# Optimization experiments

Hardware: AMD Instinct MI355X
Metric: run time of the kernel (lower is better)

Reference implementation:

```python
import jax, jax.numpy as jnp
from jax import lax
import numpy as np

DN = ('NHWC', 'HWIO', 'NHWC')


def setup_inputs() -> dict:
    key = jax.random.key(0)
    ks = jax.random.split(key, 4)
    B, T, H, W, Cin, Cout, K = 4, 16, 64, 64, 32, 64, 3
    x = jax.random.normal(ks[0], (B, T, H, W, Cin), dtype=jnp.float32)
    kernel = jax.random.normal(ks[1], (K, K, Cin, 4 * Cout), dtype=jnp.float32) * 0.05
    rec_kernel = jax.random.normal(ks[2], (K, K, Cout, 4 * Cout), dtype=jnp.float32) * 0.05
    bias = jnp.zeros((4 * Cout,), dtype=jnp.float32)
    gamma = jnp.ones((Cout,), dtype=jnp.float32)
    beta = jnp.zeros((Cout,), dtype=jnp.float32)
    moving_mean = jnp.zeros((Cout,), dtype=jnp.float32)
    moving_var = jnp.ones((Cout,), dtype=jnp.float32)
    return dict(x=x, kernel=kernel, rec_kernel=rec_kernel, bias=bias,
                gamma=gamma, beta=beta, moving_mean=moving_mean, moving_var=moving_var)


def _hard_sigmoid(z):
    # Keras hard_sigmoid: clip(0.2*x + 0.5, 0, 1)
    return jnp.clip(0.2 * z + 0.5, 0.0, 1.0)


def _conv(x, w):
    return lax.conv_general_dilated(x, w, (1, 1), 'SAME', dimension_numbers=DN)


def reference(x, kernel, rec_kernel, bias, gamma, beta, moving_mean, moving_var):
    B, T, H, W, Cin = x.shape
    Cout = rec_kernel.shape[2]
    # Precompute input-to-gate convs for all timesteps at once: (B*T,H,W,4C)
    gx = _conv(x.reshape(B * T, H, W, Cin), kernel) + bias
    gx = gx.reshape(B, T, H, W, 4 * Cout).transpose(1, 0, 2, 3, 4)  # (T,B,H,W,4C)

    def step(carry, gxt):
        h, c = carry
        g = gxt + _conv(h, rec_kernel)  # (B,H,W,4C)
        i, f, cc, o = jnp.split(g, 4, axis=-1)  # Keras gate order i,f,c,o
        i = _hard_sigmoid(i)
        f = _hard_sigmoid(f)
        c = f * c + i * jnp.tanh(cc)
        h = _hard_sigmoid(o) * jnp.tanh(c)
        return (h, c), h

    h0 = jnp.zeros((B, H, W, Cout), dtype=x.dtype)
    c0 = jnp.zeros((B, H, W, Cout), dtype=x.dtype)
    _, hs = lax.scan(step, (h0, c0), gx)  # (T,B,H,W,C)
    y = hs.transpose(1, 0, 2, 3, 4)  # (B,T,H,W,C)
    # BatchNorm, inference mode (training=False), eps=1e-3
    inv = gamma * lax.rsqrt(moving_var + 1e-3)
    return y * inv + (beta - moving_mean * inv)
```

## Files before the change

### kernel.cpp

```cpp
#include <hip/hip_runtime.h>
#include <math.h>

#define B_ 4
#define T_ 16
#define H_ 64
#define W_ 64
#define CIN 32
#define CO 64
#define NG 256
#define PXS 40

typedef __attribute__((ext_vector_type(8))) short bf16x8;
typedef __attribute__((ext_vector_type(4))) float f32x4;

__device__ __forceinline__ float hsig(float z) {
    return fminf(1.f, fmaxf(0.f, 0.2f * z + 0.5f));
}

__device__ __forceinline__ float ftanh(float x) {
    float e = __builtin_amdgcn_exp2f(x * 2.8853900817779268f);
    return 1.f - 2.f * __builtin_amdgcn_rcpf(e + 1.f);
}

__device__ __forceinline__ unsigned short f2bf(float f) {
    union { float f; unsigned u; } v; v.f = f;
    unsigned r = v.u + 0x7FFFu + ((v.u >> 16) & 1u);
    return (unsigned short)(r >> 16);
}

__global__ void transform_weights(const float* __restrict__ wk,
                                  const float* __restrict__ wr,
                                  unsigned short* __restrict__ wkT,
                                  unsigned short* __restrict__ wrT)
{
    int i = blockIdx.x * 256 + threadIdx.x;
    if (i < 9 * 256 * 32) {
        int k = i & 31, n = (i >> 5) & 255, kpos = i >> 13;
        wkT[i] = f2bf(wk[(kpos * 32 + k) * 256 + n]);
    }
    if (i < 9 * 2 * 256 * 32) {
        int k = i & 31, n = (i >> 5) & 255, q = (i >> 13) & 1, kpos = i >> 14;
        wrT[i] = f2bf(wr[(kpos * 64 + q * 32 + k) * 256 + n]);
    }
}

template<bool FIRST>
__global__ __launch_bounds__(512, 2)
void convlstm_step(const float* __restrict__ x,
                   const unsigned short* __restrict__ wkT,
                   const unsigned short* __restrict__ wrT,
                   const float* __restrict__ bias,
                   const float* __restrict__ gamma,
                   const float* __restrict__ beta,
                   const float* __restrict__ mean,
                   const float* __restrict__ var,
                   const unsigned short* __restrict__ hin,
                   unsigned short* __restrict__ hout,
                   float* __restrict__ cbuf,
                   float* __restrict__ out,
                   int t)
{
    __shared__ __align__(16) unsigned short sx[6 * 18 * PXS];
    __shared__ __align__(16) unsigned short shm[2][6 * 18 * PXS];
    __shared__ __align__(16) float axx[4 * 4 * 4 * 16 * 20];

    const int tid = threadIdx.x;
    const int wv = tid >> 6, lane = tid & 63;
    const int ln = lane & 15, kg = lane >> 4;
    const bool hwave = (wv < 4);
    const int sl = wv & 3;

    const int bi = blockIdx.x;
    const int b = bi >> 6, tile = bi & 63;
    const int oy = (tile >> 2) * 4;
    const int ox = (tile & 3) * 16;

    unsigned short* sh0 = shm[0];
    unsigned short* sh1 = shm[1];

    if (!hwave) {
#pragma unroll
        for (int i = 0; i < 2; ++i) {
            int e = (tid - 256) + i * 256;
            if (e < 432) {
                int c8 = e & 3, p = e >> 2;
                int row = p / 18, col = p - row * 18;
                int gy = oy - 1 + row, gx = ox - 1 + col;
                float4 v0 = make_float4(0.f, 0.f, 0.f, 0.f), v1 = v0;
                if ((unsigned)gy < (unsigned)H_ && (unsigned)gx < (unsigned)W_) {
                    const float* p32 = &x[((((size_t)b * T_ + t) * H_ + gy) * W_ + gx) * CIN + c8 * 8];
                    v0 = *(const float4*)p32; v1 = *(const float4*)(p32 + 4);
                }
                unsigned short* d = &sx[(row * 18 + col) * PXS + c8 * 8];
                d[0] = f2bf(v0.x); d[1] = f2bf(v0.y); d[2] = f2bf(v0.z); d[3] = f2bf(v0.w);
                d[4] = f2bf(v1.x); d[5] = f2bf(v1.y); d[6] = f2bf(v1.z); d[7] = f2bf(v1.w);
            }
        }
    } else if (!FIRST) {
#pragma unroll
        for (int i = 0; i < 4; ++i) {
            int e = tid + i * 256;
            if (e < 864) {
                int o = e & 7, p = e >> 3;
                int row = p / 18, col = p - row * 18;
                int gy = oy - 1 + row, gx = ox - 1 + col;
                uint4 v = make_uint4(0u, 0u, 0u, 0u);
                if ((unsigned)gy < (unsigned)H_ && (unsigned)gx < (unsigned)W_)
                    v = *(const uint4*)&hin[(((size_t)b * H_ + gy) * W_ + gx) * CO + o * 8];
                int q = o >> 2, s4 = o & 3;
                *(uint4*)&shm[q][(row * 18 + col) * PXS + s4 * 8] = v;
            }
        }
    }

    const int nbase = sl * 16 + ln;
    const int ch = nbase;
    const unsigned short* wkp = wkT + (size_t)nbase * 32 + kg * 8;
    const unsigned short* wrp = wrT + (size_t)nbase * 32 + kg * 8;

    const int rbase = hwave ? 0 : 2;
    const float bi0 = bias[ch], bi1 = bias[64 + ch], bi2 = bias[128 + ch], bi3 = bias[192 + ch];
    const float inv = gamma[ch] * rsqrtf(var[ch] + 1e-3f);
    const float shift = beta[ch] - mean[ch] * inv;
    float cprev[2][4];
    if (!FIRST) {
#pragma unroll
        for (int rr = 0; rr < 2; ++rr)
#pragma unroll
            for (int reg = 0; reg < 4; ++reg) {
                size_t pix = ((size_t)b * H_ + oy + rbase + rr) * W_ + (ox + kg * 4 + reg);
                cprev[rr][reg] = cbuf[pix * CO + ch];
            }
    } else {
#pragma unroll
        for (int rr = 0; rr < 2; ++rr)
#pragma unroll
            for (int reg = 0; reg < 4; ++reg) cprev[rr][reg] = 0.f;
    }

    __syncthreads();

    f32x4 acc[4][4];
#pragma unroll
    for (int g = 0; g < 4; ++g)
#pragma unroll
        for (int r = 0; r < 4; ++r) acc[g][r] = (f32x4){0.f, 0.f, 0.f, 0.f};

#define XW_WP(i)  ((i) < 9 ? (wkp + (size_t)(i) * 8192) : (wrp + (size_t)(((i) - 9) * 2 + 1) * 8192))
#define XW_SB(i)  ((i) < 9 ? sx : sh1)
#define XW_KQ(i)  ((i) < 9 ? (i) : (i) - 9)
#define HW_WP(i)  ((i) < 9 ? (wrp + (size_t)((i) * 2) * 8192) : (wrp + (size_t)(((i) - 4) * 2 + 1) * 8192))
#define HW_SB(i)  ((i) < 9 ? sh0 : sh1)
#define HW_KQ(i)  ((i) < 9 ? (i) : (i) - 4)

#define LOADW(dst, wp) { const unsigned short* wp_ = (wp);        \
    dst[0] = *(const bf16x8*)(wp_);                               \
    dst[1] = *(const bf16x8*)(wp_ + 2048);                        \
    dst[2] = *(const bf16x8*)(wp_ + 4096);                        \
    dst[3] = *(const bf16x8*)(wp_ + 6144); }

#define COMPUTE(i, SBM, KQM, BUF) {                               \
    const int kq_ = KQM(i);                                       \
    const int ky_ = kq_ / 3, kx_ = kq_ - ky_ * 3;                 \
    const unsigned short* sb_ = SBM(i);                           \
    bf16x8 a[4];                                                  \
    _Pragma("unroll")                                             \
    for (int r = 0; r < 4; ++r)                                   \
        a[r] = *(const bf16x8*)&sb_[((r + ky_) * 18 + ln + kx_) * PXS + kg * 8]; \
    __builtin_amdgcn_s_setprio(1);                                \
    _Pragma("unroll")                                             \
    for (int g = 0; g < 4; ++g)                                   \
        _Pragma("unroll")                                         \
        for (int r = 0; r < 4; ++r)                               \
            acc[g][r] = __builtin_amdgcn_mfma_f32_16x16x32_bf16(a[r], BUF[g], acc[g][r], 0, 0, 0); \
    __builtin_amdgcn_s_setprio(0); }

    if (!hwave) {
        constexpr int NCX = FIRST ? 9 : 14;
        bf16x8 P0[4], P1[4], P2[4], P3[4];
        LOADW(P0, XW_WP(0)); LOADW(P1, XW_WP(1)); LOADW(P2, XW_WP(2));
#define XSTEP(i, CUR, NXT)                                        \
        if ((i) < NCX) {                                          \
            if ((i) + 3 < NCX) LOADW(NXT, XW_WP((i) + 3));        \
            COMPUTE(i, XW_SB, XW_KQ, CUR);                        \
        }
        XSTEP(0,  P0, P3)  XSTEP(1,  P1, P0)  XSTEP(2,  P2, P1)  XSTEP(3,  P3, P2)
        XSTEP(4,  P0, P3)  XSTEP(5,  P1, P0)  XSTEP(6,  P2, P1)  XSTEP(7,  P3, P2)
        XSTEP(8,  P0, P3)  XSTEP(9,  P1, P0)  XSTEP(10, P2, P1)  XSTEP(11, P3, P2)
        XSTEP(12, P0, P3)  XSTEP(13, P1, P0)
#undef XSTEP
    } else if (!FIRST) {
        constexpr int NCH = 13;
        bf16x8 P0[4], P1[4], P2[4], P3[4];
        LOADW(P0, HW_WP(0)); LOADW(P1, HW_WP(1)); LOADW(P2, HW_WP(2));
#define HSTEP(i, CUR, NXT)                                        \
        if ((i) < NCH) {                                          \
            if ((i) + 3 < NCH) LOADW(NXT, HW_WP((i) + 3));        \
            COMPUTE(i, HW_SB, HW_KQ, CUR);                        \
        }
        HSTEP(0,  P0, P3)  HSTEP(1,  P1, P0)  HSTEP(2,  P2, P1)  HSTEP(3,  P3, P2)
        HSTEP(4,  P0, P3)  HSTEP(5,  P1, P0)  HSTEP(6,  P2, P1)  HSTEP(7,  P3, P2)
        HSTEP(8,  P0, P3)  HSTEP(9,  P1, P0)  HSTEP(10, P2, P1)  HSTEP(11, P3, P2)
        HSTEP(12, P0, P3)
#undef HSTEP
    }

    if (!hwave) {
#pragma unroll
        for (int g = 0; g < 4; ++g) {
            *(f32x4*)&axx[((((sl * 4 + g) * 4 + 0) * 16) + ln) * 20 + kg * 4] = acc[g][0];
            *(f32x4*)&axx[((((sl * 4 + g) * 4 + 1) * 16) + ln) * 20 + kg * 4] = acc[g][1];
        }
    } else {
#pragma unroll
        for (int g = 0; g < 4; ++g) {
            *(f32x4*)&axx[((((sl * 4 + g) * 4 + 2) * 16) + ln) * 20 + kg * 4] = acc[g][2];
            *(f32x4*)&axx[((((sl * 4 + g) * 4 + 3) * 16) + ln) * 20 + kg * 4] = acc[g][3];
        }
    }
    __syncthreads();

#define EPILOG(R, RR) {                                                          \
        const int gy = oy + (R);                                                 \
        f32x4 av[4];                                                             \
        _Pragma("unroll")                                                        \
        for (int g = 0; g < 4; ++g) {                                            \
            f32x4 v = *(const f32x4*)&axx[((((sl * 4 + g) * 4 + (R)) * 16) + ln) * 20 + kg * 4]; \
            av[g] = acc[g][R] + v;                                               \
        }                                                                        \
        _Pragma("unroll")                                                        \
        for (int reg = 0; reg < 4; ++reg) {                                      \
            const int gx = ox + kg * 4 + reg;                                    \
            size_t pix = ((size_t)b * H_ + gy) * W_ + gx;                        \
            float ig = hsig(av[0][reg] + bi0);                                   \
            float fg = hsig(av[1][reg] + bi1);                                   \
            float cg = ftanh(av[2][reg] + bi2);                                  \
            float og = hsig(av[3][reg] + bi3);                                   \
            float cv = fg * cprev[RR][reg] + ig * cg;                            \
            float hv = og * ftanh(cv);                                           \
            cbuf[pix * CO + ch] = cv;                                            \
            hout[pix * CO + ch] = f2bf(hv);                                      \
            __builtin_nontemporal_store(hv * inv + shift,                        \
                &out[((((size_t)b * T_ + t) * H_ + gy) * W_ + gx) * CO + ch]);   \
        }                                                                        \
    }

    if (hwave) { EPILOG(0, 0) EPILOG(1, 1) }
    else       { EPILOG(2, 0) EPILOG(3, 1) }
#undef EPILOG
}

extern "C" void kernel_launch(void* const* d_in, const int* in_sizes, int n_in,
                              void* d_out, int out_size, void* d_ws, size_t ws_size,
                              hipStream_t stream)
{
    (void)in_sizes; (void)n_in; (void)out_size; (void)ws_size;
    const float* x     = (const float*)d_in[0];
    const float* wk    = (const float*)d_in[1];
    const float* wr    = (const float*)d_in[2];
    const float* bias  = (const float*)d_in[3];
    const float* gamma = (const float*)d_in[4];
    const float* beta  = (const float*)d_in[5];
    const float* mean  = (const float*)d_in[6];
    const float* var   = (const float*)d_in[7];
    float* out = (float*)d_out;

    const size_t plane = (size_t)B_ * H_ * W_ * CO;
    unsigned short* h0 = (unsigned short*)d_ws;
    unsigned short* h1 = h0 + plane;
    float* cb = (float*)(h1 + plane);
    unsigned short* wkT = (unsigned short*)(cb + plane);
    unsigned short* wrT = wkT + 9 * 256 * 32;

    transform_weights<<<576, 256, 0, stream>>>(wk, wr, wkT, wrT);

    for (int t = 0; t < T_; ++t) {
        const unsigned short* hin = (t & 1) ? h0 : h1;
        unsigned short* houtp     = (t & 1) ? h1 : h0;
        if (t == 0)
            convlstm_step<true><<<256, 512, 0, stream>>>(x, wkT, wrT, bias, gamma, beta, mean, var,
                                                         hin, houtp, cb, out, t);
        else
            convlstm_step<false><<<256, 512, 0, stream>>>(x, wkT, wrT, bias, gamma, beta, mean, var,
                                                          hin, houtp, cb, out, t);
    }
}
```

Measured before the change: 277.8 us.

## Split K-reduction across three wave groups with LDS partial-sum exchange

Changes the block from 8 to 12 waves so the 27 K-chunks (9 input-conv, 18 recurrent-conv) split evenly into three groups of 9. Partial accumulators are exchanged through a larger LDS buffer and the epilogue rows are redistributed across the groups. The explicit 3-deep software prefetch of weights is dropped in favour of straight-line chunk loads. The aim is to balance MFMA work across waves and raise wave-level parallelism per block. In exchange it uses more LDS, tighter register limits from the new launch bounds, and an uneven epilogue, since group 0 handles two rows while the others handle one.

```diff
diff --git a/kernel.cpp b/kernel.cpp
--- a/kernel.cpp
+++ b/kernel.cpp
@@ -45,7 +45,7 @@
 }
 
 template<bool FIRST>
-__global__ __launch_bounds__(512, 2)
+__global__ __launch_bounds__(768, 3)
 void convlstm_step(const float* __restrict__ x,
                    const unsigned short* __restrict__ wkT,
                    const unsigned short* __restrict__ wrT,
@@ -62,12 +62,12 @@
 {
     __shared__ __align__(16) unsigned short sx[6 * 18 * PXS];
     __shared__ __align__(16) unsigned short shm[2][6 * 18 * PXS];
-    __shared__ __align__(16) float axx[4 * 4 * 4 * 16 * 20];
+    __shared__ __align__(16) float axx[4 * 4 * 8 * 256];
 
     const int tid = threadIdx.x;
     const int wv = tid >> 6, lane = tid & 63;
     const int ln = lane & 15, kg = lane >> 4;
-    const bool hwave = (wv < 4);
+    const int wg = wv >> 2;
     const int sl = wv & 3;
 
     const int bi = blockIdx.x;
@@ -78,10 +78,10 @@
     unsigned short* sh0 = shm[0];
     unsigned short* sh1 = shm[1];
 
-    if (!hwave) {
+    if (wg == 2) {
 #pragma unroll
         for (int i = 0; i < 2; ++i) {
-            int e = (tid - 256) + i * 256;
+            int e = (tid - 512) + i * 256;
             if (e < 432) {
                 int c8 = e & 3, p = e >> 2;
                 int row = p / 18, col = p - row * 18;
@@ -98,8 +98,8 @@
         }
     } else if (!FIRST) {
 #pragma unroll
-        for (int i = 0; i < 4; ++i) {
-            int e = tid + i * 256;
+        for (int i = 0; i < 2; ++i) {
+            int e = tid + i * 512;
             if (e < 864) {
                 int o = e & 7, p = e >> 3;
                 int row = p / 18, col = p - row * 18;
@@ -113,121 +113,114 @@
         }
     }
 
-    const int nbase = sl * 16 + ln;
-    const int ch = nbase;
-    const unsigned short* wkp = wkT + (size_t)nbase * 32 + kg * 8;
-    const unsigned short* wrp = wrT + (size_t)nbase * 32 + kg * 8;
-
-    const int rbase = hwave ? 0 : 2;
+    const int ch = sl * 16 + ln;
+    const unsigned short* wkp = wkT + (size_t)ch * 32 + kg * 8;
+    const unsigned short* wrp = wrT + (size_t)ch * 32 + kg * 8;
+
     const float bi0 = bias[ch], bi1 = bias[64 + ch], bi2 = bias[128 + ch], bi3 = bias[192 + ch];
     const float inv = gamma[ch] * rsqrtf(var[ch] + 1e-3f);
     const float shift = beta[ch] - mean[ch] * inv;
-    float cprev[2][4];
+    float cpv[2][4];
+#pragma unroll
+    for (int rr = 0; rr < 2; ++rr)
+#pragma unroll
+        for (int reg = 0; reg < 4; ++reg) cpv[rr][reg] = 0.f;
     if (!FIRST) {
-#pragma unroll
-        for (int rr = 0; rr < 2; ++rr)
+        if (wg == 0) {
 #pragma unroll
             for (int reg = 0; reg < 4; ++reg) {
-                size_t pix = ((size_t)b * H_ + oy + rbase + rr) * W_ + (ox + kg * 4 + reg);
-                cprev[rr][reg] = cbuf[pix * CO + ch];
-            }
+                size_t pix0 = ((size_t)b * H_ + oy + 0) * W_ + (ox + kg * 4 + reg);
+                size_t pix1 = ((size_t)b * H_ + oy + 1) * W_ + (ox + kg * 4 + reg);
+                cpv[0][reg] = cbuf[pix0 * CO + ch];
+                cpv[1][reg] = cbuf[pix1 * CO + ch];
+            }
+        } else {
+            const int r = (wg == 1) ? 2 : 3;
+#pragma unroll
+            for (int reg = 0; reg < 4; ++reg) {
+                size_t pix = ((size_t)b * H_ + oy + r) * W_ + (ox + kg * 4 + reg);
+                cpv[0][reg] = cbuf[pix * CO + ch];
+            }
+        }
+    }
+
+    __syncthreads();
+
+    f32x4 acc[4][4];
+#pragma unroll
+    for (int g = 0; g < 4; ++g)
+#pragma unroll
+        for (int r = 0; r < 4; ++r) acc[g][r] = (f32x4){0.f, 0.f, 0.f, 0.f};
+
+#define WPTR(c) ((c) < 9 ? (wkp + (size_t)(c) * 8192) : (wrp + (size_t)((c) - 9) * 8192))
+#define SRCB(c) ((c) < 9 ? sx : ((((c) - 9) & 1) ? sh1 : sh0))
+#define KP(c)   ((c) < 9 ? (c) : (((c) - 9) >> 1))
+
+#define CHUNK(c) {                                                               \
+    const unsigned short* wp_ = WPTR(c);                                         \
+    bf16x8 w0 = *(const bf16x8*)(wp_);                                           \
+    bf16x8 w1 = *(const bf16x8*)(wp_ + 2048);                                    \
+    bf16x8 w2 = *(const bf16x8*)(wp_ + 4096);                                    \
+    bf16x8 w3 = *(const bf16x8*)(wp_ + 6144);                                    \
+    const int ky_ = KP(c) / 3, kx_ = KP(c) - (KP(c) / 3) * 3;                    \
+    const unsigned short* sb_ = SRCB(c);                                         \
+    bf16x8 a0 = *(const bf16x8*)&sb_[((0 + ky_) * 18 + ln + kx_) * PXS + kg * 8];\
+    bf16x8 a1 = *(const bf16x8*)&sb_[((1 + ky_) * 18 + ln + kx_) * PXS + kg * 8];\
+    bf16x8 a2 = *(const bf16x8*)&sb_[((2 + ky_) * 18 + ln + kx_) * PXS + kg * 8];\
+    bf16x8 a3 = *(const bf16x8*)&sb_[((3 + ky_) * 18 + ln + kx_) * PXS + kg * 8];\
+    __builtin_amdgcn_s_setprio(1);                                               \
+    acc[0][0] = __builtin_amdgcn_mfma_f32_16x16x32_bf16(a0, w0, acc[0][0], 0, 0, 0); \
+    acc[0][1] = __builtin_amdgcn_mfma_f32_16x16x32_bf16(a1, w0, acc[0][1], 0, 0, 0); \
+    acc[0][2] = __builtin_amdgcn_mfma_f32_16x16x32_bf16(a2, w0, acc[0][2], 0, 0, 0); \
+    acc[0][3] = __builtin_amdgcn_mfma_f32_16x16x32_bf16(a3, w0, acc[0][3], 0, 0, 0); \
+    acc[1][0] = __builtin_amdgcn_mfma_f32_16x16x32_bf16(a0, w1, acc[1][0], 0, 0, 0); \
+    acc[1][1] = __builtin_amdgcn_mfma_f32_16x16x32_bf16(a1, w1, acc[1][1], 0, 0, 0); \
+    acc[1][2] = __builtin_amdgcn_mfma_f32_16x16x32_bf16(a2, w1, acc[1][2], 0, 0, 0); \
+    acc[1][3] = __builtin_amdgcn_mfma_f32_16x16x32_bf16(a3, w1, acc[1][3], 0, 0, 0); \
+    acc[2][0] = __builtin_amdgcn_mfma_f32_16x16x32_bf16(a0, w2, acc[2][0], 0, 0, 0); \
+    acc[2][1] = __builtin_amdgcn_mfma_f32_16x16x32_bf16(a1, w2, acc[2][1], 0, 0, 0); \
+    acc[2][2] = __builtin_amdgcn_mfma_f32_16x16x32_bf16(a2, w2, acc[2][2], 0, 0, 0); \
+    acc[2][3] = __builtin_amdgcn_mfma_f32_16x16x32_bf16(a3, w2, acc[2][3], 0, 0, 0); \
+    acc[3][0] = __builtin_amdgcn_mfma_f32_16x16x32_bf16(a0, w3, acc[3][0], 0, 0, 0); \
+    acc[3][1] = __builtin_amdgcn_mfma_f32_16x16x32_bf16(a1, w3, acc[3][1], 0, 0, 0); \
+    acc[3][2] = __builtin_amdgcn_mfma_f32_16x16x32_bf16(a2, w3, acc[3][2], 0, 0, 0); \
+    acc[3][3] = __builtin_amdgcn_mfma_f32_16x16x32_bf16(a3, w3, acc[3][3], 0, 0, 0); \
+    __builtin_amdgcn_s_setprio(0); }
+
+    if (wg == 0) {
+        CHUNK(0) CHUNK(1) CHUNK(2) CHUNK(3) CHUNK(4) CHUNK(5) CHUNK(6) CHUNK(7) CHUNK(8)
+    } else if (wg == 1) {
+        if (!FIRST) {
+            CHUNK(9) CHUNK(10) CHUNK(11) CHUNK(12) CHUNK(13) CHUNK(14) CHUNK(15) CHUNK(16) CHUNK(17)
+        }
     } else {
-#pragma unroll
-        for (int rr = 0; rr < 2; ++rr)
-#pragma unroll
-            for (int reg = 0; reg < 4; ++reg) cprev[rr][reg] = 0.f;
-    }
-
+        if (!FIRST) {
+            CHUNK(18) CHUNK(19) CHUNK(20) CHUNK(21) CHUNK(22) CHUNK(23) CHUNK(24) CHUNK(25) CHUNK(26)
+        }
+    }
+
+    const int axo = (ln << 4) + (kg << 2);
+#define AXPUB(s, G, R) *(f32x4*)&axx[(((sl * 4 + (G)) * 8 + (s)) << 8) + axo] = acc[G][R];
+#define AXRD(s, G)     (*(const f32x4*)&axx[(((sl * 4 + (G)) * 8 + (s)) << 8) + axo])
+
+    if (wg == 0) {
+#pragma unroll
+        for (int g = 0; g < 4; ++g) { AXPUB(4, g, 2) AXPUB(6, g, 3) }
+    } else if (wg == 1) {
+#pragma unroll
+        for (int g = 0; g < 4; ++g) { AXPUB(0, g, 0) AXPUB(2, g, 1) AXPUB(7, g, 3) }
+    } else {
+#pragma unroll
+        for (int g = 0; g < 4; ++g) { AXPUB(1, g, 0) AXPUB(3, g, 1) AXPUB(5, g, 2) }
+    }
     __syncthreads();
 
-    f32x4 acc[4][4];
-#pragma unroll
-    for (int g = 0; g < 4; ++g)
-#pragma unroll
-        for (int r = 0; r < 4; ++r) acc[g][r] = (f32x4){0.f, 0.f, 0.f, 0.f};
-
-#define XW_WP(i)  ((i) < 9 ? (wkp + (size_t)(i) * 8192) : (wrp + (size_t)(((i) - 9) * 2 + 1) * 8192))
-#define XW_SB(i)  ((i) < 9 ? sx : sh1)
-#define XW_KQ(i)  ((i) < 9 ? (i) : (i) - 9)
-#define HW_WP(i)  ((i) < 9 ? (wrp + (size_t)((i) * 2) * 8192) : (wrp + (size_t)(((i) - 4) * 2 + 1) * 8192))
-#define HW_SB(i)  ((i) < 9 ? sh0 : sh1)
-#define HW_KQ(i)  ((i) < 9 ? (i) : (i) - 4)
-
-#define LOADW(dst, wp) { const unsigned short* wp_ = (wp);        \
-    dst[0] = *(const bf16x8*)(wp_);                               \
-    dst[1] = *(const bf16x8*)(wp_ + 2048);                        \
-    dst[2] = *(const bf16x8*)(wp_ + 4096);                        \
-    dst[3] = *(const bf16x8*)(wp_ + 6144); }
-
-#define COMPUTE(i, SBM, KQM, BUF) {                               \
-    const int kq_ = KQM(i);                                       \
-    const int ky_ = kq_ / 3, kx_ = kq_ - ky_ * 3;                 \
-    const unsigned short* sb_ = SBM(i);                           \
-    bf16x8 a[4];                                                  \
-    _Pragma("unroll")                                             \
-    for (int r = 0; r < 4; ++r)                                   \
-        a[r] = *(const bf16x8*)&sb_[((r + ky_) * 18 + ln + kx_) * PXS + kg * 8]; \
-    __builtin_amdgcn_s_setprio(1);                                \
-    _Pragma("unroll")                                             \
-    for (int g = 0; g < 4; ++g)                                   \
-        _Pragma("unroll")                                         \
-        for (int r = 0; r < 4; ++r)                               \
-            acc[g][r] = __builtin_amdgcn_mfma_f32_16x16x32_bf16(a[r], BUF[g], acc[g][r], 0, 0, 0); \
-    __builtin_amdgcn_s_setprio(0); }
-
-    if (!hwave) {
-        constexpr int NCX = FIRST ? 9 : 14;
-        bf16x8 P0[4], P1[4], P2[4], P3[4];
-        LOADW(P0, XW_WP(0)); LOADW(P1, XW_WP(1)); LOADW(P2, XW_WP(2));
-#define XSTEP(i, CUR, NXT)                                        \
-        if ((i) < NCX) {                                          \
-            if ((i) + 3 < NCX) LOADW(NXT, XW_WP((i) + 3));        \
-            COMPUTE(i, XW_SB, XW_KQ, CUR);                        \
-        }
-        XSTEP(0,  P0, P3)  XSTEP(1,  P1, P0)  XSTEP(2,  P2, P1)  XSTEP(3,  P3, P2)
-        XSTEP(4,  P0, P3)  XSTEP(5,  P1, P0)  XSTEP(6,  P2, P1)  XSTEP(7,  P3, P2)
-        XSTEP(8,  P0, P3)  XSTEP(9,  P1, P0)  XSTEP(10, P2, P1)  XSTEP(11, P3, P2)
-        XSTEP(12, P0, P3)  XSTEP(13, P1, P0)
-#undef XSTEP
-    } else if (!FIRST) {
-        constexpr int NCH = 13;
-        bf16x8 P0[4], P1[4], P2[4], P3[4];
-        LOADW(P0, HW_WP(0)); LOADW(P1, HW_WP(1)); LOADW(P2, HW_WP(2));
-#define HSTEP(i, CUR, NXT)                                        \
-        if ((i) < NCH) {                                          \
-            if ((i) + 3 < NCH) LOADW(NXT, HW_WP((i) + 3));        \
-            COMPUTE(i, HW_SB, HW_KQ, CUR);                        \
-        }
-        HSTEP(0,  P0, P3)  HSTEP(1,  P1, P0)  HSTEP(2,  P2, P1)  HSTEP(3,  P3, P2)
-        HSTEP(4,  P0, P3)  HSTEP(5,  P1, P0)  HSTEP(6,  P2, P1)  HSTEP(7,  P3, P2)
-        HSTEP(8,  P0, P3)  HSTEP(9,  P1, P0)  HSTEP(10, P2, P1)  HSTEP(11, P3, P2)
-        HSTEP(12, P0, P3)
-#undef HSTEP
-    }
-
-    if (!hwave) {
-#pragma unroll
-        for (int g = 0; g < 4; ++g) {
-            *(f32x4*)&axx[((((sl * 4 + g) * 4 + 0) * 16) + ln) * 20 + kg * 4] = acc[g][0];
-            *(f32x4*)&axx[((((sl * 4 + g) * 4 + 1) * 16) + ln) * 20 + kg * 4] = acc[g][1];
-        }
-    } else {
-#pragma unroll
-        for (int g = 0; g < 4; ++g) {
-            *(f32x4*)&axx[((((sl * 4 + g) * 4 + 2) * 16) + ln) * 20 + kg * 4] = acc[g][2];
-            *(f32x4*)&axx[((((sl * 4 + g) * 4 + 3) * 16) + ln) * 20 + kg * 4] = acc[g][3];
-        }
-    }
-    __syncthreads();
-
-#define EPILOG(R, RR) {                                                          \
+#define EPI(R, CPI, S0, S1) {                                                    \
         const int gy = oy + (R);                                                 \
         f32x4 av[4];                                                             \
         _Pragma("unroll")                                                        \
-        for (int g = 0; g < 4; ++g) {                                            \
-            f32x4 v = *(const f32x4*)&axx[((((sl * 4 + g) * 4 + (R)) * 16) + ln) * 20 + kg * 4]; \
-            av[g] = acc[g][R] + v;                                               \
-        }                                                                        \
+        for (int g = 0; g < 4; ++g)                                              \
+            av[g] = acc[g][R] + AXRD(S0, g) + AXRD(S1, g);                       \
         _Pragma("unroll")                                                        \
         for (int reg = 0; reg < 4; ++reg) {                                      \
             const int gx = ox + kg * 4 + reg;                                    \
@@ -236,7 +229,7 @@
             float fg = hsig(av[1][reg] + bi1);                                   \
             float cg = ftanh(av[2][reg] + bi2);                                  \
             float og = hsig(av[3][reg] + bi3);                                   \
-            float cv = fg * cprev[RR][reg] + ig * cg;                            \
+            float cv = fg * cpv[CPI][reg] + ig * cg;                             \
             float hv = og * ftanh(cv);                                           \
             cbuf[pix * CO + ch] = cv;                                            \
             hout[pix * CO + ch] = f2bf(hv);                                      \
@@ -245,9 +238,16 @@
         }                                                                        \
     }
 
-    if (hwave) { EPILOG(0, 0) EPILOG(1, 1) }
-    else       { EPILOG(2, 0) EPILOG(3, 1) }
-#undef EPILOG
+    if (wg == 0)      { EPI(0, 0, 0, 1) EPI(1, 1, 2, 3) }
+    else if (wg == 1) { EPI(2, 0, 4, 5) }
+    else              { EPI(3, 0, 6, 7) }
+#undef EPI
+#undef AXPUB
+#undef AXRD
+#undef CHUNK
+#undef WPTR
+#undef SRCB
+#undef KP
 }
 
 extern "C" void kernel_launch(void* const* d_in, const int* in_sizes, int n_in,
@@ -278,10 +278,10 @@
         const unsigned short* hin = (t & 1) ? h0 : h1;
         unsigned short* houtp     = (t & 1) ? h1 : h0;
         if (t == 0)
-            convlstm_step<true><<<256, 512, 0, stream>>>(x, wkT, wrT, bias, gamma, beta, mean, var,
+            convlstm_step<true><<<256, 768, 0, stream>>>(x, wkT, wrT, bias, gamma, beta, mean, var,
                                                          hin, houtp, cb, out, t);
         else
-            convlstm_step<false><<<256, 512, 0, stream>>>(x, wkT, wrT, bias, gamma, beta, mean, var,
+            convlstm_step<false><<<256, 768, 0, stream>>>(x, wkT, wrT, bias, gamma, beta, mean, var,
                                                           hin, houtp, cb, out, t);
     }
 }
```

New measurement: 294.9 us. 1.06x slower.
